# Kernel tuning notes

Hardware: AMD Instinct MI355X
Metric: run time of the kernel (lower is better)

Reference implementation:

```python
import jax, jax.numpy as jnp
import numpy as np

L = 6        # num_coupling_layers
T_DIM = 64   # t_dim
HALF = T_DIM // 2
COND = 128   # cond_dim
HID = 1024   # hidden_dim
B = 32768


def setup_inputs() -> dict:
    key = jax.random.key(0)
    ks = jax.random.split(key, 8)
    s_in = 1.0 / np.sqrt(HALF + COND)
    s_h = 1.0 / np.sqrt(HID)
    T = jax.random.normal(ks[0], (B, T_DIM), dtype=jnp.float32)
    cond = jax.random.normal(ks[1], (B, COND), dtype=jnp.float32)
    W1 = jax.random.normal(ks[2], (L, HALF + COND, HID), dtype=jnp.float32) * s_in
    b1 = jnp.zeros((L, HID), dtype=jnp.float32)
    W2 = jax.random.normal(ks[3], (L, HID, HID), dtype=jnp.float32) * s_h
    b2 = jnp.zeros((L, HID), dtype=jnp.float32)
    W3 = jax.random.normal(ks[4], (L, HID, 2 * HALF), dtype=jnp.float32) * s_h
    b3 = jnp.zeros((L, 2 * HALF), dtype=jnp.float32)
    return {"T": T, "cond": cond, "W1": W1, "b1": b1, "W2": W2, "b2": b2, "W3": W3, "b3": b3}


def reference(T, cond, W1, b1, W2, b2, W3, b3):
    # Conditional normalizing flow: 6 affine coupling layers with alternating
    # contiguous half masks. Even layers transform the first half, odd the second.
    def mlp(h, i):
        x = jax.nn.relu(h @ W1[i] + b1[i])
        x = jax.nn.relu(x @ W2[i] + b2[i])
        return x @ W3[i] + b3[i]

    z = T
    log_det = jnp.zeros(T.shape[0], dtype=T.dtype)
    for i in range(L):
        if i % 2 == 0:
            masked, unmasked = z[:, :HALF], z[:, HALF:]
        else:
            masked, unmasked = z[:, HALF:], z[:, :HALF]
        params = mlp(jnp.concatenate([unmasked, cond], axis=1), i)
        s = jnp.tanh(params[:, :HALF])
        t_shift = params[:, HALF:]
        y_masked = masked * jnp.exp(s) + t_shift
        if i % 2 == 0:
            z = jnp.concatenate([y_masked, unmasked], axis=1)
        else:
            z = jnp.concatenate([unmasked, y_masked], axis=1)
        log_det = log_det + jnp.sum(s, axis=1)
    return z, log_det
```

## Files before the change

kernel.cpp:

```cpp
#include <hip/hip_runtime.h>
#include <hip/hip_fp16.h>
#include <stdint.h>

typedef _Float16 f16;
typedef _Float16 f16x8 __attribute__((ext_vector_type(8)));
typedef float f32x4 __attribute__((ext_vector_type(4)));

#define NB 32768
#define LAYERS 6
#define AK 160
#define HID 1024

__device__ __forceinline__ void async_copy16(const void* g, void* l) {
  __builtin_amdgcn_global_load_lds(
      (const __attribute__((address_space(1))) void*)g,
      (__attribute__((address_space(3))) void*)l, 16, 0, 0);
}

__device__ __forceinline__ void wtrans_tile(const float* __restrict__ W,
                                            f16* __restrict__ Wt,
                                            const int K_, const int N_,
                                            const int bx, const int by,
                                            const int bz, float (*t)[65])
{
  const long off = (long)bz * K_ * N_;
  const float* Wl = W + off;
  f16* Wtl = Wt + off;
  const int k0 = by * 64, n0 = bx * 64;
  const int tx = threadIdx.x & 63, ty4 = threadIdx.x >> 6;
#pragma unroll
  for (int r = ty4; r < 64; r += 4) {
    const int k = k0 + r;
    if (k < K_) t[r][tx] = Wl[(long)k * N_ + n0 + tx];
  }
  __syncthreads();
  const int k = k0 + tx;
  if (k < K_) {
#pragma unroll
    for (int r = ty4; r < 64; r += 4) {
      const int n = n0 + r;
      Wtl[(long)n * K_ + k] = (f16)t[tx][r];
    }
  }
}

__global__ void prep_all(const float* __restrict__ T, const float* __restrict__ cond,
                         const float* __restrict__ W1, const float* __restrict__ W2,
                         const float* __restrict__ W3,
                         float* __restrict__ z, float* __restrict__ ld,
                         f16* __restrict__ A,
                         f16* __restrict__ W1t, f16* __restrict__ W2t,
                         f16* __restrict__ W3t)
{
  __shared__ float t[64][65];
  const int b = blockIdx.x;
  if (b < 2048) {
    const int S1 = NB * 64;
    const int S2 = S1 + NB;
    const int S3 = S2 + NB * 32;
    const int S4 = S3 + NB * 128;
    for (int i = b * blockDim.x + threadIdx.x; i < S4; i += 2048 * blockDim.x) {
      if (i < S1) {
        z[i] = T[i];
      } else if (i < S2) {
        ld[i - S1] = 0.0f;
      } else if (i < S3) {
        int r = i - S2;
        int row = r >> 5, j = r & 31;
        A[(size_t)row * AK + j] = (f16)T[row * 64 + 32 + j];
      } else {
        int r = i - S3;
        int row = r >> 7, j = r & 127;
        A[(size_t)row * AK + 32 + j] = (f16)cond[r];
      }
    }
  } else if (b < 2048 + 288) {
    const int l = b - 2048;
    wtrans_tile(W1, W1t, AK, 1024, l % 16, (l / 16) % 3, l / 48, t);
  } else if (b < 2048 + 288 + 1536) {
    const int l = b - (2048 + 288);
    wtrans_tile(W2, W2t, HID, 1024, l % 16, (l / 16) % 16, l / 256, t);
  } else {
    const int l = b - (2048 + 288 + 1536);
    wtrans_tile(W3, W3t, HID, 64, 0, l % 16, l / 16, t);
  }
}

__global__ __launch_bounds__(256, 2)
void gemm1_full(const f16* __restrict__ A,
                const f16* __restrict__ Wt,
                const float* __restrict__ bias,
                f16* __restrict__ C)
{
  __shared__ __align__(16) f16 As[128 * 160];
  __shared__ __align__(16) f16 Bs[128 * 160];
  const int tid  = threadIdx.x;
  const int lane = tid & 63;
  const int wave = tid >> 6;
  const int c15  = lane & 15;
  const int quad = lane >> 4;
  const int wm = (wave & 1) * 64;
  const int wn = (wave >> 1) * 64;

  const int b = blockIdx.x;
  const int x = b & 7, i = b >> 3;
  const long rowStart = (long)(x * 32 + (i >> 3)) * 128;
  const long colStart = (long)(i & 7) * 128;

  const f16* Ab = A  + rowStart * AK;
  const f16* Bb = Wt + colStart * AK;

#pragma unroll
  for (int it = 0; it < 10; ++it) {
    const int f = it * 256 + tid;
    const int row = f / 20;
    const int ch  = f - row * 20;
    const int chs = ch ^ ((row >> 1) & 3);
    async_copy16(Ab + (long)row * AK + chs * 8, &As[0] + (long)f * 8);
    async_copy16(Bb + (long)row * AK + chs * 8, &Bs[0] + (long)f * 8);
  }
  __syncthreads();

  f32x4 acc[4][4] = {};
#pragma unroll
  for (int kt = 0; kt < 5; ++kt) {
    f16x8 a[4], bf[4];
#pragma unroll
    for (int mi = 0; mi < 4; ++mi) {
      const int R = wm + mi * 16 + c15;
      a[mi] = *(const f16x8*)&As[(R * 20 + kt * 4 + (quad ^ ((R >> 1) & 3))) * 8];
    }
#pragma unroll
    for (int ni = 0; ni < 4; ++ni) {
      const int R = wn + ni * 16 + c15;
      bf[ni] = *(const f16x8*)&Bs[(R * 20 + kt * 4 + (quad ^ ((R >> 1) & 3))) * 8];
    }
#pragma unroll
    for (int mi = 0; mi < 4; ++mi)
#pragma unroll
      for (int ni = 0; ni < 4; ++ni)
        acc[mi][ni] = __builtin_amdgcn_mfma_f32_16x16x32_f16(
            a[mi], bf[ni], acc[mi][ni], 0, 0, 0);
  }

#pragma unroll
  for (int ni = 0; ni < 4; ++ni) {
    const long gn = colStart + wn + ni * 16 + c15;
    const float bv = bias[gn];
#pragma unroll
    for (int mi = 0; mi < 4; ++mi) {
#pragma unroll
      for (int r = 0; r < 4; ++r) {
        const long gm = rowStart + wm + mi * 16 + quad * 4 + r;
        float v = acc[mi][ni][r] + bv;
        v = fmaxf(v, 0.0f);
        C[gm * HID + gn] = (f16)v;
      }
    }
  }
}

__global__ __launch_bounds__(256, 4)
void gemm12(const f16* __restrict__ A, const int K,
            const f16* __restrict__ Wt,
            const float* __restrict__ bias,
            f16* __restrict__ C)
{
  __shared__ __align__(16) f16 As[2][128 * 32];
  __shared__ __align__(16) f16 Bs[2][128 * 32];
  const int tid  = threadIdx.x;
  const int wave = tid >> 6;
  const int lane = tid & 63;
  const int c15  = lane & 15;
  const int quad = lane >> 4;
  const int wm = (wave & 1) * 64;
  const int wn = (wave >> 1) * 64;

  const int b = blockIdx.x;
  const int x = b & 7, i = b >> 3;
  const long rowStart = (long)(x * 32 + (i >> 3)) * 128;
  const long colStart = (long)(i & 7) * 128;

  const f16* Ab = A  + rowStart * K;
  const f16* Bb = Wt + colStart * K;

  const int ra  = tid >> 2;
  const int kca = (((tid & 3) ^ ((ra >> 1) & 3))) * 8;

  f32x4 acc[4][4] = {};
  const int nK = K >> 5;

  auto stage = [&](int kt, int sel) {
    const long ko = (long)kt * 32;
    f16* as = &As[sel][0];
    f16* bs = &Bs[sel][0];
#pragma unroll
    for (int q = 0; q < 2; ++q)
      async_copy16(Ab + (long)(q * 64 + ra) * K + ko + kca,
                   as + (q * 256 + wave * 64) * 8);
#pragma unroll
    for (int q = 0; q < 2; ++q)
      async_copy16(Bb + (long)(q * 64 + ra) * K + ko + kca,
                   bs + (q * 256 + wave * 64) * 8);
  };

  stage(0, 0);
  for (int kt = 0; kt < nK; ++kt) {
    __syncthreads();
    if (kt + 1 < nK) stage(kt + 1, (kt + 1) & 1);
    const f16* as = &As[kt & 1][0];
    const f16* bs = &Bs[kt & 1][0];

    f16x8 a[4], bf[4];
#pragma unroll
    for (int mi = 0; mi < 4; ++mi) {
      const int R = wm + mi * 16 + c15;
      a[mi] = *(const f16x8*)&as[R * 32 + ((quad ^ ((R >> 1) & 3)) << 3)];
    }
#pragma unroll
    for (int ni = 0; ni < 4; ++ni) {
      const int R = wn + ni * 16 + c15;
      bf[ni] = *(const f16x8*)&bs[R * 32 + ((quad ^ ((R >> 1) & 3)) << 3)];
    }
#pragma unroll
    for (int mi = 0; mi < 4; ++mi)
#pragma unroll
      for (int ni = 0; ni < 4; ++ni)
        acc[mi][ni] = __builtin_amdgcn_mfma_f32_16x16x32_f16(
            a[mi], bf[ni], acc[mi][ni], 0, 0, 0);
  }

#pragma unroll
  for (int ni = 0; ni < 4; ++ni) {
    const long gn = colStart + wn + ni * 16 + c15;
    const float bv = bias[gn];
#pragma unroll
    for (int mi = 0; mi < 4; ++mi) {
#pragma unroll
      for (int r = 0; r < 4; ++r) {
        const long gm = rowStart + wm + mi * 16 + quad * 4 + r;
        float v = acc[mi][ni][r] + bv;
        v = fmaxf(v, 0.0f);
        C[gm * HID + gn] = (f16)v;
      }
    }
  }
}

__global__ __launch_bounds__(256, 4)
void gemm3_coupling(const f16* __restrict__ X2, const f16* __restrict__ W3t,
                    const float* __restrict__ b3, float* __restrict__ z,
                    float* __restrict__ log_det, f16* __restrict__ Anext,
                    const int maskoff)
{
  __shared__ __align__(16) f16 As[2][64 * 32];
  __shared__ __align__(16) f16 Bs[2][64 * 32];
  const int tid = threadIdx.x;
  const int wave = tid >> 6, lane = tid & 63;
  const int c15 = lane & 15, quad = lane >> 4;
  const int wm = wave * 16;
  const long rowStart = (long)blockIdx.x * 64;

  const f16* Ab = X2 + rowStart * HID;
  const int ra  = tid >> 2;
  const int kca = (((tid & 3) ^ ((ra >> 1) & 3))) * 8;

  f32x4 acc[4] = {};

  auto stage = [&](int kt, int sel) {
    const long ko = (long)kt * 32;
    async_copy16(Ab + (long)ra * HID + ko + kca,
                 &As[sel][0] + (wave * 64) * 8);
    async_copy16(W3t + (long)ra * HID + ko + kca,
                 &Bs[sel][0] + (wave * 64) * 8);
  };

  stage(0, 0);
  for (int kt = 0; kt < 32; ++kt) {
    __syncthreads();
    if (kt + 1 < 32) stage(kt + 1, (kt + 1) & 1);
    const f16* as = &As[kt & 1][0];
    const f16* bs = &Bs[kt & 1][0];

    const int Ra = wm + c15;
    f16x8 a = *(const f16x8*)&as[Ra * 32 + ((quad ^ ((Ra >> 1) & 3)) << 3)];
    f16x8 bf[4];
#pragma unroll
    for (int ni = 0; ni < 4; ++ni) {
      const int R = ni * 16 + c15;
      bf[ni] = *(const f16x8*)&bs[R * 32 + ((quad ^ ((R >> 1) & 3)) << 3)];
    }
#pragma unroll
    for (int ni = 0; ni < 4; ++ni)
      acc[ni] = __builtin_amdgcn_mfma_f32_16x16x32_f16(a, bf[ni], acc[ni], 0, 0, 0);
  }

  float sp[4] = {0.0f, 0.0f, 0.0f, 0.0f};
#pragma unroll
  for (int ni = 0; ni < 2; ++ni) {
    const int j = ni * 16 + c15;
    const float bs = b3[j];
    const float bt = b3[32 + j];
#pragma unroll
    for (int r = 0; r < 4; ++r) {
      const long gm = rowStart + wm + quad * 4 + r;
      const float sv = acc[ni][r] + bs;
      const float e2 = __expf(2.0f * sv);
      const float s  = 1.0f - 2.0f / (e2 + 1.0f);
      const float tv = acc[ni + 2][r] + bt;
      const float m  = z[gm * 64 + maskoff + j];
      const float y  = fmaf(m, __expf(s), tv);
      z[gm * 64 + maskoff + j] = y;
      Anext[gm * AK + j] = (f16)y;
      sp[r] += s;
    }
  }
#pragma unroll
  for (int r = 0; r < 4; ++r) {
    float v = sp[r];
    v += __shfl_xor(v, 1);
    v += __shfl_xor(v, 2);
    v += __shfl_xor(v, 4);
    v += __shfl_xor(v, 8);
    if (c15 == 0) {
      const long gm = rowStart + wm + quad * 4 + r;
      log_det[gm] += v;
    }
  }
}

extern "C" void kernel_launch(void* const* d_in, const int* in_sizes, int n_in,
                              void* d_out, int out_size, void* d_ws, size_t ws_size,
                              hipStream_t stream) {
  (void)in_sizes; (void)n_in; (void)out_size; (void)ws_size;
  const float* T    = (const float*)d_in[0];
  const float* cond = (const float*)d_in[1];
  const float* W1   = (const float*)d_in[2];
  const float* b1   = (const float*)d_in[3];
  const float* W2   = (const float*)d_in[4];
  const float* b2   = (const float*)d_in[5];
  const float* W3   = (const float*)d_in[6];
  const float* b3   = (const float*)d_in[7];

  float* z  = (float*)d_out;
  float* ld = z + (size_t)NB * 64;

  f16* A   = (f16*)d_ws;
  f16* X1  = A   + (size_t)NB * AK;
  f16* X2  = X1  + (size_t)NB * HID;
  f16* W1t = X2  + (size_t)NB * HID;
  f16* W2t = W1t + (size_t)6 * 1024 * 160;
  f16* W3t = W2t + ((size_t)6 << 20);

  prep_all<<<3968, 256, 0, stream>>>(T, cond, W1, W2, W3,
                                     z, ld, A, W1t, W2t, W3t);

  const int g12 = (NB / 128) * (HID / 128);
  for (int l = 0; l < LAYERS; ++l) {
    gemm1_full<<<g12, 256, 0, stream>>>(A, W1t + (size_t)l * 1024 * AK,
                                        b1 + l * 1024, X1);
    gemm12<<<g12, 256, 0, stream>>>(X1, HID, W2t + ((size_t)l << 20),
                                    b2 + l * 1024, X2);
    const int maskoff = (l & 1) ? 32 : 0;
    gemm3_coupling<<<NB / 64, 256, 0, stream>>>(X2, W3t + (size_t)l * 64 * 1024,
                                                b3 + l * 64, z, ld, A, maskoff);
  }
}
```

Before: 875.7 us.

## Use producer-consumer warp specialization with triple-buffered LDS ring for hidden GEMM

Replaces the double-buffered hidden-layer GEMM with a kernel that adds a fifth wave acting as a dedicated loader. That wave fills a three-slot LDS ring with async global-to-LDS copies, and four compute waves consume the slots. Block-wide barriers are replaced by per-slot flag and consumed counters polled with atomics and s_sleep. This aims to hide load latency and remove barrier stalls, at the cost of spin-wait overhead, 48KB of LDS per block and the loss of the 4-blocks-per-CU launch bound, which may reduce occupancy.

```diff
diff --git a/kernel.cpp b/kernel.cpp
--- a/kernel.cpp
+++ b/kernel.cpp
@@ -160,56 +160,79 @@
   }
 }
 
-__global__ __launch_bounds__(256, 4)
-void gemm12(const f16* __restrict__ A, const int K,
-            const f16* __restrict__ Wt,
-            const float* __restrict__ bias,
-            f16* __restrict__ C)
-{
-  __shared__ __align__(16) f16 As[2][128 * 32];
-  __shared__ __align__(16) f16 Bs[2][128 * 32];
+__global__ __launch_bounds__(320)
+void gemm2_pc(const f16* __restrict__ A,
+              const f16* __restrict__ Wt,
+              const float* __restrict__ bias,
+              f16* __restrict__ C)
+{
+  __shared__ __align__(16) f16 ring[3][8192];
+  __shared__ int flag[3];
+  __shared__ int consumed[3];
+
   const int tid  = threadIdx.x;
   const int wave = tid >> 6;
   const int lane = tid & 63;
+
+  const int b = blockIdx.x;
+  const int x = b & 7, i = b >> 3;
+  const long rowStart = (long)(x * 32 + (i >> 3)) * 128;
+  const long colStart = (long)(i & 7) * 128;
+  const int K = HID, nK = 32;
+
+  if (tid < 3) { flag[tid] = 0; consumed[tid] = 0; }
+  __syncthreads();
+
+  if (wave == 4) {
+    const f16* Ab = A  + rowStart * K;
+    const f16* Bb = Wt + colStart * K;
+    const int rowA = lane >> 2;
+    const int kc   = ((lane & 3) ^ ((rowA >> 1) & 3)) * 8;
+    for (int kt = 0; kt < nK; ++kt) {
+      const int slot = kt % 3;
+      if (kt >= 3) {
+        const int want = 4 * (kt / 3);
+        while (__hip_atomic_load(&consumed[slot], __ATOMIC_RELAXED,
+                                 __HIP_MEMORY_SCOPE_WORKGROUP) < want)
+          __builtin_amdgcn_s_sleep(1);
+      }
+      const long ko = (long)kt * 32;
+      f16* as = &ring[slot][0];
+      f16* bs = &ring[slot][4096];
+#pragma unroll
+      for (int is = 0; is < 8; ++is) {
+        const int row = is * 16 + rowA;
+        const int kcs = ((lane & 3) ^ ((row >> 1) & 3)) * 8;
+        async_copy16(Ab + (long)row * K + ko + kcs, as + (is * 64) * 8);
+        async_copy16(Bb + (long)row * K + ko + kcs, bs + (is * 64) * 8);
+      }
+      if (kt >= 1) {
+        asm volatile("s_waitcnt vmcnt(16)" ::: "memory");
+        __hip_atomic_store(&flag[(kt - 1) % 3], kt, __ATOMIC_RELEASE,
+                           __HIP_MEMORY_SCOPE_WORKGROUP);
+      }
+    }
+    asm volatile("s_waitcnt vmcnt(0)" ::: "memory");
+    __hip_atomic_store(&flag[(nK - 1) % 3], nK, __ATOMIC_RELEASE,
+                       __HIP_MEMORY_SCOPE_WORKGROUP);
+    (void)kc;
+    return;
+  }
+
   const int c15  = lane & 15;
   const int quad = lane >> 4;
   const int wm = (wave & 1) * 64;
   const int wn = (wave >> 1) * 64;
 
-  const int b = blockIdx.x;
-  const int x = b & 7, i = b >> 3;
-  const long rowStart = (long)(x * 32 + (i >> 3)) * 128;
-  const long colStart = (long)(i & 7) * 128;
-
-  const f16* Ab = A  + rowStart * K;
-  const f16* Bb = Wt + colStart * K;
-
-  const int ra  = tid >> 2;
-  const int kca = (((tid & 3) ^ ((ra >> 1) & 3))) * 8;
-
   f32x4 acc[4][4] = {};
-  const int nK = K >> 5;
-
-  auto stage = [&](int kt, int sel) {
-    const long ko = (long)kt * 32;
-    f16* as = &As[sel][0];
-    f16* bs = &Bs[sel][0];
-#pragma unroll
-    for (int q = 0; q < 2; ++q)
-      async_copy16(Ab + (long)(q * 64 + ra) * K + ko + kca,
-                   as + (q * 256 + wave * 64) * 8);
-#pragma unroll
-    for (int q = 0; q < 2; ++q)
-      async_copy16(Bb + (long)(q * 64 + ra) * K + ko + kca,
-                   bs + (q * 256 + wave * 64) * 8);
-  };
-
-  stage(0, 0);
+
   for (int kt = 0; kt < nK; ++kt) {
-    __syncthreads();
-    if (kt + 1 < nK) stage(kt + 1, (kt + 1) & 1);
-    const f16* as = &As[kt & 1][0];
-    const f16* bs = &Bs[kt & 1][0];
+    const int slot = kt % 3;
+    while (__hip_atomic_load(&flag[slot], __ATOMIC_ACQUIRE,
+                             __HIP_MEMORY_SCOPE_WORKGROUP) < kt + 1)
+      __builtin_amdgcn_s_sleep(1);
+    const f16* as = &ring[slot][0];
+    const f16* bs = &ring[slot][4096];
 
     f16x8 a[4], bf[4];
 #pragma unroll
@@ -228,6 +251,10 @@
       for (int ni = 0; ni < 4; ++ni)
         acc[mi][ni] = __builtin_amdgcn_mfma_f32_16x16x32_f16(
             a[mi], bf[ni], acc[mi][ni], 0, 0, 0);
+
+    if (lane == 0)
+      __hip_atomic_fetch_add(&consumed[slot], 1, __ATOMIC_RELEASE,
+                             __HIP_MEMORY_SCOPE_WORKGROUP);
   }
 
 #pragma unroll
@@ -359,8 +386,8 @@
   for (int l = 0; l < LAYERS; ++l) {
     gemm1_full<<<g12, 256, 0, stream>>>(A, W1t + (size_t)l * 1024 * AK,
                                         b1 + l * 1024, X1);
-    gemm12<<<g12, 256, 0, stream>>>(X1, HID, W2t + ((size_t)l << 20),
-                                    b2 + l * 1024, X2);
+    gemm2_pc<<<g12, 320, 0, stream>>>(X1, W2t + ((size_t)l << 20),
+                                      b2 + l * 1024, X2);
     const int maskoff = (l & 1) ? 32 : 0;
     gemm3_coupling<<<NB / 64, 256, 0, stream>>>(X2, W3t + (size_t)l * 64 * 1024,
                                                 b3 + l * 64, z, ld, A, maskoff);
```

New measurement: 951.0 us. 1.09x slower.

## Fuse coupling-layer GEMM3 epilogue with next layer's GEMM1 in one kernel

Applied to the files above, without the earlier changes.

Adds a g3g1 kernel that computes the W3 projection and affine coupling update for a 64-row tile, then reuses the freshly written A rows from LDS to compute the next layer's first MLP GEMM (bias+ReLU) into X1. This removes five separate gemm1 launches and a re-read of A per layer. The fused kernel uses more LDS and only 64-row tiles with 2-wave occupancy bound, so the GEMM1 portion has less reuse of W1 than the prior 128x128 tiling. gemm12's launch bounds are also lowered from 4 to 3 blocks per SM.

```diff
diff --git a/kernel.cpp b/kernel.cpp
--- a/kernel.cpp
+++ b/kernel.cpp
@@ -160,7 +160,7 @@
   }
 }
 
-__global__ __launch_bounds__(256, 4)
+__global__ __launch_bounds__(256, 3)
 void gemm12(const f16* __restrict__ A, const int K,
             const f16* __restrict__ Wt,
             const float* __restrict__ bias,
@@ -247,6 +247,169 @@
   }
 }
 
+__global__ __launch_bounds__(256, 2)
+void g3g1(const f16* __restrict__ X2, const f16* __restrict__ W3t,
+          const float* __restrict__ b3, float* __restrict__ z,
+          float* __restrict__ log_det, f16* __restrict__ A,
+          const int maskoff,
+          const f16* __restrict__ W1n,
+          const float* __restrict__ b1n,
+          f16* __restrict__ X1)
+{
+  __shared__ __align__(16) f16 As3[2][64 * 32];
+  __shared__ __align__(16) f16 Bs3[2][64 * 32];
+  __shared__ __align__(16) f16 smA[64 * 160];
+  __shared__ __align__(16) f16 smB[2][128 * 32];
+
+  const int tid = threadIdx.x;
+  const int wave = tid >> 6, lane = tid & 63;
+  const int c15 = lane & 15, quad = lane >> 4;
+  const long rowStart = (long)blockIdx.x * 64;
+
+  {
+    const int wm = wave * 16;
+    const f16* Ab = X2 + rowStart * HID;
+    const int ra  = tid >> 2;
+    const int kca = (((tid & 3) ^ ((ra >> 1) & 3))) * 8;
+
+    f32x4 acc[4] = {};
+
+    auto stage = [&](int kt, int sel) {
+      const long ko = (long)kt * 32;
+      async_copy16(Ab + (long)ra * HID + ko + kca,
+                   &As3[sel][0] + (wave * 64) * 8);
+      async_copy16(W3t + (long)ra * HID + ko + kca,
+                   &Bs3[sel][0] + (wave * 64) * 8);
+    };
+
+    stage(0, 0);
+    for (int kt = 0; kt < 32; ++kt) {
+      __syncthreads();
+      if (kt + 1 < 32) stage(kt + 1, (kt + 1) & 1);
+      const f16* as = &As3[kt & 1][0];
+      const f16* bs = &Bs3[kt & 1][0];
+
+      const int Ra = wm + c15;
+      f16x8 a = *(const f16x8*)&as[Ra * 32 + ((quad ^ ((Ra >> 1) & 3)) << 3)];
+      f16x8 bf[4];
+#pragma unroll
+      for (int ni = 0; ni < 4; ++ni) {
+        const int R = ni * 16 + c15;
+        bf[ni] = *(const f16x8*)&bs[R * 32 + ((quad ^ ((R >> 1) & 3)) << 3)];
+      }
+#pragma unroll
+      for (int ni = 0; ni < 4; ++ni)
+        acc[ni] = __builtin_amdgcn_mfma_f32_16x16x32_f16(a, bf[ni], acc[ni], 0, 0, 0);
+    }
+
+    float sp[4] = {0.0f, 0.0f, 0.0f, 0.0f};
+#pragma unroll
+    for (int ni = 0; ni < 2; ++ni) {
+      const int j = ni * 16 + c15;
+      const float bs = b3[j];
+      const float bt = b3[32 + j];
+#pragma unroll
+      for (int r = 0; r < 4; ++r) {
+        const long gm = rowStart + wm + quad * 4 + r;
+        const float sv = acc[ni][r] + bs;
+        const float e2 = __expf(2.0f * sv);
+        const float s  = 1.0f - 2.0f / (e2 + 1.0f);
+        const float tv = acc[ni + 2][r] + bt;
+        const float m  = z[gm * 64 + maskoff + j];
+        const float y  = fmaf(m, __expf(s), tv);
+        z[gm * 64 + maskoff + j] = y;
+        A[gm * AK + j] = (f16)y;
+        sp[r] += s;
+      }
+    }
+#pragma unroll
+    for (int r = 0; r < 4; ++r) {
+      float v = sp[r];
+      v += __shfl_xor(v, 1);
+      v += __shfl_xor(v, 2);
+      v += __shfl_xor(v, 4);
+      v += __shfl_xor(v, 8);
+      if (c15 == 0) {
+        const long gm = rowStart + wm + quad * 4 + r;
+        log_det[gm] += v;
+      }
+    }
+  }
+
+  __syncthreads();
+
+  {
+#pragma unroll
+    for (int it = 0; it < 5; ++it) {
+      const int f = it * 256 + tid;
+      const int row = f / 20;
+      const int ch  = f - row * 20;
+      const int chs = ch ^ ((row >> 1) & 3);
+      async_copy16(A + (rowStart + row) * AK + chs * 8, &smA[0] + (long)f * 8);
+    }
+
+    const int ra  = tid >> 2;
+    const int kca = (((tid & 3) ^ ((ra >> 1) & 3))) * 8;
+    const int wm1 = (wave & 1) * 32;
+    const int wn  = (wave >> 1) * 64;
+
+    auto stageB = [&](int s, int sel) {
+      const int ct = s / 5, kt = s - ct * 5;
+      const f16* Bb = W1n + (long)(ct * 128) * AK;
+#pragma unroll
+      for (int q = 0; q < 2; ++q)
+        async_copy16(Bb + (long)(q * 64 + ra) * AK + kt * 32 + kca,
+                     &smB[sel][0] + (q * 256 + wave * 64) * 8);
+    };
+
+    stageB(0, 0);
+    f32x4 acc1[2][4] = {};
+    for (int s = 0; s < 40; ++s) {
+      __syncthreads();
+      if (s + 1 < 40) stageB(s + 1, (s + 1) & 1);
+      const int ct = s / 5, kt = s - ct * 5;
+      const f16* bs = &smB[s & 1][0];
+
+      f16x8 a[2], bf[4];
+#pragma unroll
+      for (int mi = 0; mi < 2; ++mi) {
+        const int R = wm1 + mi * 16 + c15;
+        a[mi] = *(const f16x8*)&smA[(R * 20 + kt * 4 + (quad ^ ((R >> 1) & 3))) * 8];
+      }
+#pragma unroll
+      for (int ni = 0; ni < 4; ++ni) {
+        const int R = wn + ni * 16 + c15;
+        bf[ni] = *(const f16x8*)&bs[R * 32 + ((quad ^ ((R >> 1) & 3)) << 3)];
+      }
+#pragma unroll
+      for (int mi = 0; mi < 2; ++mi)
+#pragma unroll
+        for (int ni = 0; ni < 4; ++ni)
+          acc1[mi][ni] = __builtin_amdgcn_mfma_f32_16x16x32_f16(
+              a[mi], bf[ni], acc1[mi][ni], 0, 0, 0);
+
+      if (kt == 4) {
+#pragma unroll
+        for (int ni = 0; ni < 4; ++ni) {
+          const long gn = (long)ct * 128 + wn + ni * 16 + c15;
+          const float bv = b1n[gn];
+#pragma unroll
+          for (int mi = 0; mi < 2; ++mi) {
+#pragma unroll
+            for (int r = 0; r < 4; ++r) {
+              const long gm = rowStart + wm1 + mi * 16 + quad * 4 + r;
+              float v = acc1[mi][ni][r] + bv;
+              v = fmaxf(v, 0.0f);
+              X1[gm * HID + gn] = (f16)v;
+              acc1[mi][ni][r] = 0.0f;
+            }
+          }
+        }
+      }
+    }
+  }
+}
+
 __global__ __launch_bounds__(256, 4)
 void gemm3_coupling(const f16* __restrict__ X2, const f16* __restrict__ W3t,
                     const float* __restrict__ b3, float* __restrict__ z,
@@ -356,13 +519,19 @@
                                      z, ld, A, W1t, W2t, W3t);
 
   const int g12 = (NB / 128) * (HID / 128);
+  gemm1_full<<<g12, 256, 0, stream>>>(A, W1t, b1, X1);
+
   for (int l = 0; l < LAYERS; ++l) {
-    gemm1_full<<<g12, 256, 0, stream>>>(A, W1t + (size_t)l * 1024 * AK,
-                                        b1 + l * 1024, X1);
     gemm12<<<g12, 256, 0, stream>>>(X1, HID, W2t + ((size_t)l << 20),
                                     b2 + l * 1024, X2);
     const int maskoff = (l & 1) ? 32 : 0;
-    gemm3_coupling<<<NB / 64, 256, 0, stream>>>(X2, W3t + (size_t)l * 64 * 1024,
-                                                b3 + l * 64, z, ld, A, maskoff);
-  }
-}
+    if (l < LAYERS - 1) {
+      g3g1<<<NB / 64, 256, 0, stream>>>(
+          X2, W3t + (size_t)l * 64 * 1024, b3 + l * 64, z, ld, A, maskoff,
+          W1t + (size_t)(l + 1) * 1024 * AK, b1 + (l + 1) * 1024, X1);
+    } else {
+      gemm3_coupling<<<NB / 64, 256, 0, stream>>>(
+          X2, W3t + (size_t)l * 64 * 1024, b3 + l * 64, z, ld, A, maskoff);
+    }
+  }
+}
```

Measured after the change: 885.5 us. No clear change (+1.1%).
